# Kernel optimization log

Hardware: AMD Instinct MI355X
Metric: run time of the kernel (lower is better)

## Reference

```python
import jax, jax.numpy as jnp
import numpy as np

N = 50000      # nodes
E = 800000     # edges (avg degree 16)
G = 50         # graphs in batch (1000 nodes each)
D_IN, H, H2, OUT = 8, 128, 64, 1


def setup_inputs() -> dict:
    key = jax.random.key(0)
    ks = jax.random.split(key, 16)
    src = jax.random.randint(ks[0], (E,), 0, N)
    # every node gets at least one in-edge (forward computes 3/in_deg)
    dst = jnp.concatenate([jnp.arange(N), jax.random.randint(ks[1], (E - N,), 0, N)])
    graph_ids = jnp.arange(N) // (N // G)

    def lin(k, fan_in, fan_out):
        return jax.random.normal(k, (fan_in, fan_out), jnp.float32) / np.float32(np.sqrt(fan_in))

    inp = {"src": src, "dst": dst, "graph_ids": graph_ids}
    dims = [(D_IN, H), (H, H), (H, H), (H, H), (H, H)]
    for i, (fi, fo) in enumerate(dims):
        inp[f"W{i+1}"] = lin(ks[2 + i], fi, fo)
        inp[f"b{i+1}"] = jnp.zeros((fo,), jnp.float32)
    inp["lw1"] = lin(ks[8], H, H2)
    inp["lb1"] = jnp.zeros((H2,), jnp.float32)
    inp["lw2"] = lin(ks[9], H2, OUT)
    inp["lb2"] = jnp.zeros((OUT,), jnp.float32)
    return inp


def reference(src, dst, graph_ids, W1, b1, W2, b2, W3, b3, W4, b4, W5, b5, lw1, lb1, lw2, lb2):
    ones_e = jnp.ones((E,), jnp.float32)
    in_deg = jax.ops.segment_sum(ones_e, dst, num_segments=N)   # [N]
    out_deg = jax.ops.segment_sum(ones_e, src, num_segments=N)  # [N]

    # degree features (8 channels)
    h1 = in_deg[:, None]
    h2 = (in_deg > 3.0).astype(jnp.float32)[:, None]
    h3 = 3.0 / h1
    h4 = (in_deg > 4.0).astype(jnp.float32)[:, None]
    h_ = jnp.concatenate([h1, h2, h3, h4, -h1, -h2, -h3, -h4], axis=1)  # [N,8]

    # DGL GraphConv norm='both': clamp degrees to min 1 for normalization
    norm_src = jnp.maximum(out_deg, 1.0) ** -0.5  # [N]
    norm_dst = jnp.maximum(in_deg, 1.0) ** -0.5   # [N]

    def conv(h, W, b):
        m = (h * norm_src[:, None])[src]                        # [E, d] gather
        agg = jax.ops.segment_sum(m, dst, num_segments=N)       # [N, d] scatter-add
        return agg * norm_dst[:, None] @ W + b

    h_co = jax.nn.relu(conv(h_, W1, b1))
    h_co = jax.nn.relu(conv(h_co, W2, b2))
    h_co = jax.nn.relu(conv(h_co, W3, b3))
    h_co = jax.nn.relu(conv(h_co, W4, b4))
    h_co = jax.nn.relu(conv(h_co, W5, b5))                      # [N, H]

    # dgl.mean_nodes: per-graph mean pool
    counts = jax.ops.segment_sum(jnp.ones((N,), jnp.float32), graph_ids, num_segments=G)
    graph_emb = jax.ops.segment_sum(h_co, graph_ids, num_segments=G) / counts[:, None]  # [G, H]

    # dropout layers are identity in eval mode
    h_emb = jax.nn.relu(graph_emb @ lw1 + lb1)
    pred = jax.nn.sigmoid(h_emb @ lw2 + lb2)                    # [G, 1]
    return (pred, graph_emb, h_co)
```

## Files before the change

### kernel.cpp

```cpp
#include <hip/hip_runtime.h>
#include <math.h>

#define N_NODES 50000
#define N_EDGES 800000
#define N_GRAPHS 50
#define HD 128
#define TM 64
#define LDA 68
#define POOL_CHUNK 125
#define SCAN_B 256
#define SCAN_NB ((N_NODES + SCAN_B - 1) / SCAN_B)
#define NB_H 128
#define CH_H (N_EDGES / NB_H)
#define NBIN2 (N_NODES / 2)

__global__ __launch_bounds__(256) void k_hist(const int* __restrict__ src,
                                              const int* __restrict__ dst,
                                              unsigned* __restrict__ part_in,
                                              unsigned* __restrict__ part_out) {
    __shared__ unsigned cnt[NBIN2];
    int t = threadIdx.x, b = blockIdx.x;
    int e0 = b * CH_H;
    for (int j = t; j < NBIN2; j += 256) cnt[j] = 0;
    __syncthreads();
    for (int e = e0 + t; e < e0 + CH_H; e += 256) {
        int i = dst[e];
        atomicAdd(&cnt[i >> 1], 1u << ((i & 1) * 16));
    }
    __syncthreads();
    for (int j = t; j < NBIN2; j += 256) part_in[b * NBIN2 + j] = cnt[j];
    __syncthreads();
    for (int j = t; j < NBIN2; j += 256) cnt[j] = 0;
    __syncthreads();
    for (int e = e0 + t; e < e0 + CH_H; e += 256) {
        int i = src[e];
        atomicAdd(&cnt[i >> 1], 1u << ((i & 1) * 16));
    }
    __syncthreads();
    for (int j = t; j < NBIN2; j += 256) part_out[b * NBIN2 + j] = cnt[j];
}

__global__ void k_dreduce(const unsigned* __restrict__ part_in,
                          const unsigned* __restrict__ part_out,
                          int* __restrict__ deg_in, int* __restrict__ deg_out) {
    int j = blockIdx.x * blockDim.x + threadIdx.x;
    if (j >= NBIN2) return;
    unsigned ilo = 0, ihi = 0, olo = 0, ohi = 0;
#pragma unroll 4
    for (int b = 0; b < NB_H; ++b) {
        unsigned pi = part_in[b * NBIN2 + j];
        unsigned po = part_out[b * NBIN2 + j];
        ilo += pi & 0xFFFFu; ihi += pi >> 16;
        olo += po & 0xFFFFu; ohi += po >> 16;
    }
    ((int2*)deg_in)[j] = make_int2((int)ilo, (int)ihi);
    ((int2*)deg_out)[j] = make_int2((int)olo, (int)ohi);
}

__global__ void k_norms(const int* __restrict__ deg_in, const int* __restrict__ deg_out,
                        const int* __restrict__ gids,
                        float* norm_src, float* norm_dst, int* gcount,
                        float4* __restrict__ feat4) {
    __shared__ int hist[N_GRAPHS];
    int t = threadIdx.x;
    if (t < N_GRAPHS) hist[t] = 0;
    __syncthreads();
    int i = blockIdx.x * blockDim.x + t;
    if (i < N_NODES) {
        float di = (float)deg_in[i];
        float dq = (float)deg_out[i];
        float nd = 1.0f / sqrtf(fmaxf(di, 1.0f));
        float ns = 1.0f / sqrtf(fmaxf(dq, 1.0f));
        norm_dst[i] = nd;
        norm_src[i] = ns;
        float4 f;
        f.x = di * ns;
        f.y = (di > 3.0f) ? ns : 0.0f;
        f.z = (3.0f / di) * ns;
        f.w = (di > 4.0f) ? ns : 0.0f;
        feat4[i] = f;
        atomicAdd(&hist[gids[i]], 1);
    }
    __syncthreads();
    if (t < N_GRAPHS && hist[t] != 0) atomicAdd(&gcount[t], hist[t]);
}

__global__ void k_scan1(const int* __restrict__ deg_in, int* off, int* bsum) {
    __shared__ int sh[SCAN_B];
    int t = threadIdx.x;
    int i = blockIdx.x * SCAN_B + t;
    int v = (i < N_NODES) ? deg_in[i] : 0;
    sh[t] = v;
    __syncthreads();
    for (int o = 1; o < SCAN_B; o <<= 1) {
        int u = (t >= o) ? sh[t - o] : 0;
        __syncthreads();
        sh[t] += u;
        __syncthreads();
    }
    if (i < N_NODES) off[i] = sh[t] - v;
    if (t == SCAN_B - 1) bsum[blockIdx.x] = sh[t];
}

__global__ void k_scan2(int* bsum, int* off) {
    __shared__ int sh[SCAN_B];
    int t = threadIdx.x;
    int v = (t < SCAN_NB) ? bsum[t] : 0;
    sh[t] = v;
    __syncthreads();
    for (int o = 1; o < SCAN_B; o <<= 1) {
        int u = (t >= o) ? sh[t - o] : 0;
        __syncthreads();
        sh[t] += u;
        __syncthreads();
    }
    if (t < SCAN_NB) bsum[t] = sh[t] - v;
    if (t == SCAN_B - 1) off[N_NODES] = sh[t];
}

__global__ void k_scan3(int* off, const int* __restrict__ bsum, int* cursor) {
    int b = blockIdx.x, t = threadIdx.x;
    int i = b * SCAN_B + t;
    if (i < N_NODES) {
        int o = off[i] + bsum[b];
        off[i] = o;
        cursor[i] = o;
    }
}

__global__ void k_scatter(const int* __restrict__ src, const int* __restrict__ dst,
                          int* cursor, int* csr) {
    int e = blockIdx.x * blockDim.x + threadIdx.x;
    if (e < N_EDGES) {
        int p = atomicAdd(&cursor[dst[e]], 1);
        csr[p] = src[e];
    }
}

__global__ void k_agg1(const int* __restrict__ off, const int* __restrict__ csr,
                       const float4* __restrict__ feat4,
                       const float* __restrict__ ndst, float* __restrict__ agg8) {
    int i = blockIdx.x * blockDim.x + threadIdx.x;
    if (i >= N_NODES) return;
    int e0 = off[i], e1 = off[i + 1];
    float a0 = 0.f, a1 = 0.f, a2 = 0.f, a3 = 0.f;
    int e = e0;
    for (; e + 1 < e1; e += 2) {
        float4 f0 = feat4[csr[e]];
        float4 f1 = feat4[csr[e + 1]];
        a0 += f0.x + f1.x; a1 += f0.y + f1.y;
        a2 += f0.z + f1.z; a3 += f0.w + f1.w;
    }
    if (e < e1) {
        float4 f0 = feat4[csr[e]];
        a0 += f0.x; a1 += f0.y; a2 += f0.z; a3 += f0.w;
    }
    float nd = ndst[i];
    a0 *= nd; a1 *= nd; a2 *= nd; a3 *= nd;
    float4* p = (float4*)(agg8 + (size_t)i * 8);
    float4 hi = { a0, a1, a2, a3 };
    float4 lo = { -a0, -a1, -a2, -a3 };
    p[0] = hi;
    p[1] = lo;
}

__global__ void k_gemm1(const float* __restrict__ agg8, const float* __restrict__ W,
                        const float* __restrict__ b, const float* __restrict__ nsrc,
                        float* __restrict__ out) {
    __shared__ float Wsh[8 * 128];
    int t = threadIdx.x;
    for (int i = t; i < 1024; i += 256) Wsh[i] = W[i];
    __syncthreads();
    int row = blockIdx.x * 2 + (t >> 7);
    int j = t & 127;
    if (row >= N_NODES) return;
    const float* a = agg8 + (size_t)row * 8;
    float acc = b[j];
#pragma unroll
    for (int k = 0; k < 8; ++k) acc += a[k] * Wsh[k * 128 + j];
    out[(size_t)row * HD + j] = fmaxf(acc, 0.0f) * nsrc[row];
}

__global__ void k_agg4(const int* __restrict__ off, const int* __restrict__ csr,
                       const float* __restrict__ ndst,
                       const float* __restrict__ h, float* __restrict__ out) {
    int wid = (blockIdx.x * blockDim.x + threadIdx.x) >> 6;
    int lane = threadIdx.x & 63;
    if (wid >= N_NODES) return;
    int half = lane >> 5;
    int q = lane & 31;
    int e0 = off[wid], e1 = off[wid + 1];
    float4 a = { 0.f, 0.f, 0.f, 0.f };
    int e = e0 + half;
    for (; e + 2 < e1; e += 4) {
        int s0 = csr[e], s1 = csr[e + 2];
        float4 v0 = *(const float4*)(h + (size_t)s0 * HD + q * 4);
        float4 v1 = *(const float4*)(h + (size_t)s1 * HD + q * 4);
        a.x += v0.x + v1.x; a.y += v0.y + v1.y;
        a.z += v0.z + v1.z; a.w += v0.w + v1.w;
    }
    if (e < e1) {
        int s0 = csr[e];
        float4 v0 = *(const float4*)(h + (size_t)s0 * HD + q * 4);
        a.x += v0.x; a.y += v0.y; a.z += v0.z; a.w += v0.w;
    }
    a.x += __shfl_xor(a.x, 32);
    a.y += __shfl_xor(a.y, 32);
    a.z += __shfl_xor(a.z, 32);
    a.w += __shfl_xor(a.w, 32);
    if (half == 0) {
        float nd = ndst[wid];
        a.x *= nd; a.y *= nd; a.z *= nd; a.w *= nd;
        *(float4*)(out + (size_t)wid * HD + q * 4) = a;
    }
}

__global__ void k_agg2(const int* __restrict__ off, const int* __restrict__ csr,
                       const float* __restrict__ ndst,
                       const float* __restrict__ h, float* __restrict__ out) {
    int wid = (blockIdx.x * blockDim.x + threadIdx.x) >> 6;
    int lane = threadIdx.x & 63;
    if (wid >= N_NODES) return;
    int e0 = off[wid], e1 = off[wid + 1];
    float a0 = 0.f, a1 = 0.f;
    int e = e0;
    for (; e + 3 < e1; e += 4) {
        int s0 = csr[e], s1 = csr[e + 1], s2 = csr[e + 2], s3 = csr[e + 3];
        float2 v0 = *(const float2*)(h + (size_t)s0 * HD + lane * 2);
        float2 v1 = *(const float2*)(h + (size_t)s1 * HD + lane * 2);
        float2 v2 = *(const float2*)(h + (size_t)s2 * HD + lane * 2);
        float2 v3 = *(const float2*)(h + (size_t)s3 * HD + lane * 2);
        a0 += v0.x + v1.x + v2.x + v3.x;
        a1 += v0.y + v1.y + v2.y + v3.y;
    }
    for (; e < e1; ++e) {
        int s0 = csr[e];
        float2 v0 = *(const float2*)(h + (size_t)s0 * HD + lane * 2);
        a0 += v0.x; a1 += v0.y;
    }
    float nd = ndst[wid];
    float2 o; o.x = a0 * nd; o.y = a1 * nd;
    *(float2*)(out + (size_t)wid * HD + lane * 2) = o;
}

__global__ __launch_bounds__(512) void k_gemm(const float* __restrict__ A,
                                              const float* __restrict__ W,
                                              const float* __restrict__ b,
                                              const float* __restrict__ nsrc,
                                              int premult,
                                              float* __restrict__ out) {
    __shared__ float Wsh[128 * 128];
    __shared__ float Ash[128 * LDA];
    int t = threadIdx.x;
    const float4* W4 = (const float4*)W;
    float4* Wsh4 = (float4*)Wsh;
#pragma unroll
    for (int i = 0; i < 8; ++i) Wsh4[t + i * 512] = W4[t + i * 512];
    int row0 = blockIdx.x * TM;
#pragma unroll
    for (int i = 0; i < 4; ++i) {
        int idx = t + i * 512;
        int r = idx >> 5;
        int q = idx & 31;
        int row = row0 + r;
        if (row >= N_NODES) row = N_NODES - 1;
        float4 v = ((const float4*)(A + (size_t)row * HD))[q];
        Ash[(4 * q + 0) * LDA + r] = v.x;
        Ash[(4 * q + 1) * LDA + r] = v.y;
        Ash[(4 * q + 2) * LDA + r] = v.z;
        Ash[(4 * q + 3) * LDA + r] = v.w;
    }
    __syncthreads();
    int j0 = (t & 31) * 4;
    int r0 = (t >> 5) * 4;
    float4 bv = *(const float4*)(b + j0);
    float acc[4][4];
#pragma unroll
    for (int r = 0; r < 4; ++r) {
        acc[r][0] = bv.x; acc[r][1] = bv.y; acc[r][2] = bv.z; acc[r][3] = bv.w;
    }
#pragma unroll 4
    for (int k = 0; k < 128; ++k) {
        float4 w = *(const float4*)&Wsh[k * 128 + j0];
        float4 a = *(const float4*)&Ash[k * LDA + r0];
        acc[0][0] += a.x * w.x; acc[0][1] += a.x * w.y; acc[0][2] += a.x * w.z; acc[0][3] += a.x * w.w;
        acc[1][0] += a.y * w.x; acc[1][1] += a.y * w.y; acc[1][2] += a.y * w.z; acc[1][3] += a.y * w.w;
        acc[2][0] += a.z * w.x; acc[2][1] += a.z * w.y; acc[2][2] += a.z * w.z; acc[2][3] += a.z * w.w;
        acc[3][0] += a.w * w.x; acc[3][1] += a.w * w.y; acc[3][2] += a.w * w.z; acc[3][3] += a.w * w.w;
    }
#pragma unroll
    for (int r = 0; r < 4; ++r) {
        int row = row0 + r0 + r;
        if (row < N_NODES) {
            float sc = premult ? nsrc[row] : 1.0f;
            float* op = out + (size_t)row * HD + j0;
            float2 o01 = { fmaxf(acc[r][0], 0.f) * sc, fmaxf(acc[r][1], 0.f) * sc };
            float2 o23 = { fmaxf(acc[r][2], 0.f) * sc, fmaxf(acc[r][3], 0.f) * sc };
            *(float2*)op = o01;
            *(float2*)(op + 2) = o23;
        }
    }
}

__global__ void k_pool(const float* __restrict__ hco, const int* __restrict__ gids,
                       float* gsum) {
    int f = threadIdx.x;
    int n0 = blockIdx.x * POOL_CHUNK;
    int g = gids[n0];
    float s = 0.f;
    for (int i = 0; i < POOL_CHUNK; ++i)
        s += hco[(size_t)(n0 + i) * HD + f];
    atomicAdd(&gsum[g * HD + f], s);
}

__global__ void k_head(const float* __restrict__ gsum, const int* __restrict__ gcount,
                       const float* __restrict__ lw1, const float* __restrict__ lb1,
                       const float* __restrict__ lw2, const float* __restrict__ lb2,
                       float* __restrict__ dout) {
    __shared__ float ge[128];
    int g = blockIdx.x, j = threadIdx.x;
    float cnt = (float)gcount[g];
    float g0 = gsum[g * HD + j] / cnt;
    float g1 = gsum[g * HD + 64 + j] / cnt;
    ge[j] = g0; ge[64 + j] = g1;
    dout[N_GRAPHS + g * HD + j] = g0;
    dout[N_GRAPHS + g * HD + 64 + j] = g1;
    __syncthreads();
    float acc = lb1[j];
#pragma unroll 4
    for (int k = 0; k < 128; ++k) acc += ge[k] * lw1[k * 64 + j];
    float he = fmaxf(acc, 0.f);
    float p = he * lw2[j];
#pragma unroll
    for (int o = 32; o > 0; o >>= 1) p += __shfl_down(p, o);
    if (j == 0) dout[g] = 1.0f / (1.0f + expf(-(p + lb2[0])));
}

extern "C" void kernel_launch(void* const* d_in, const int* in_sizes, int n_in,
                              void* d_out, int out_size, void* d_ws, size_t ws_size,
                              hipStream_t stream) {
    const int* src  = (const int*)d_in[0];
    const int* dst  = (const int*)d_in[1];
    const int* gids = (const int*)d_in[2];
    const float* W1 = (const float*)d_in[3];  const float* b1 = (const float*)d_in[4];
    const float* W2 = (const float*)d_in[5];  const float* b2 = (const float*)d_in[6];
    const float* W3 = (const float*)d_in[7];  const float* b3 = (const float*)d_in[8];
    const float* W4 = (const float*)d_in[9];  const float* b4 = (const float*)d_in[10];
    const float* W5 = (const float*)d_in[11]; const float* b5 = (const float*)d_in[12];
    const float* lw1 = (const float*)d_in[13]; const float* lb1 = (const float*)d_in[14];
    const float* lw2 = (const float*)d_in[15]; const float* lb2 = (const float*)d_in[16];
    float* out = (float*)d_out;

    char* ws = (char*)d_ws;
    int*    gcount   = (int*)(ws + 0);
    float*  gsum     = (float*)(ws + 256);
    const size_t ZERO_BYTES = 25856;
    int*    deg_in   = (int*)(ws + 26112);
    int*    deg_out  = (int*)(ws + 226304);
    int*    off      = (int*)(ws + 426496);
    int*    cursor   = (int*)(ws + 626688);
    int*    csr      = (int*)(ws + 826880);
    float*  norm_src = (float*)(ws + 4026880);
    float*  norm_dst = (float*)(ws + 4227072);
    int*    bsum     = (int*)(ws + 4427264);
    float4* feat4    = (float4*)(ws + 4428288);
    float*  aggbuf   = (float*)(ws + 5228544);
    float*  hws      = (float*)(ws + 30828544);
    const size_t WS_NEEDED = 30828544 + 25600000;

    unsigned* part_in  = (unsigned*)aggbuf;
    unsigned* part_out = (unsigned*)aggbuf + NB_H * NBIN2;

    float* hco = out + (N_GRAPHS + N_GRAPHS * HD);
    bool aligned = (ws_size >= WS_NEEDED);
    float* hbuf = aligned ? hws : hco;

    hipMemsetAsync(ws, 0, ZERO_BYTES, stream);

    k_hist<<<NB_H, 256, 0, stream>>>(src, dst, part_in, part_out);
    k_dreduce<<<(NBIN2 + 255) / 256, 256, 0, stream>>>(part_in, part_out,
                                                       deg_in, deg_out);
    k_norms<<<(N_NODES + 255) / 256, 256, 0, stream>>>(deg_in, deg_out, gids,
                                                       norm_src, norm_dst, gcount, feat4);
    k_scan1<<<SCAN_NB, SCAN_B, 0, stream>>>(deg_in, off, bsum);
    k_scan2<<<1, SCAN_B, 0, stream>>>(bsum, off);
    k_scan3<<<SCAN_NB, SCAN_B, 0, stream>>>(off, bsum, cursor);
    k_scatter<<<(N_EDGES + 255) / 256, 256, 0, stream>>>(src, dst, cursor, csr);

    k_agg1<<<(N_NODES + 255) / 256, 256, 0, stream>>>(off, csr, feat4, norm_dst, aggbuf);
    k_gemm1<<<N_NODES / 2, 256, 0, stream>>>(aggbuf, W1, b1, norm_src, hbuf);

    const float* Ws[4] = { W2, W3, W4, W5 };
    const float* bs[4] = { b2, b3, b4, b5 };
    for (int L = 0; L < 4; ++L) {
        if (aligned)
            k_agg4<<<(N_NODES * 64 + 255) / 256, 256, 0, stream>>>(off, csr,
                                                                   norm_dst, hbuf, aggbuf);
        else
            k_agg2<<<(N_NODES * 64 + 255) / 256, 256, 0, stream>>>(off, csr,
                                                                   norm_dst, hbuf, aggbuf);
        float* gout = (L < 3) ? hbuf : hco;
        k_gemm<<<(N_NODES + TM - 1) / TM, 512, 0, stream>>>(aggbuf, Ws[L], bs[L],
                                                            norm_src, (L < 3) ? 1 : 0,
                                                            gout);
    }

    k_pool<<<N_NODES / POOL_CHUNK, 128, 0, stream>>>(hco, gids, gsum);
    k_head<<<N_GRAPHS, 64, 0, stream>>>(gsum, gcount, lw1, lb1, lw2, lb2, out);
}
```

Before: 540.5 us.

## Build CSR from per-block histogram prefix offsets instead of global atomics

The degree-reduction kernel now writes, for each histogram block, an exclusive running prefix of the packed per-node counts back into the partial buffer. A new scatter kernel loads its block's prefix into LDS and uses shared-memory atomics to rank each edge within its destination. This replaces the global-atomic cursor scatter and drops the cursor buffer, and the CSR order becomes deterministic. The gather in the aggregation kernel is also unrolled to four loads in flight per half-wave. Risks: the 16-bit packed running sums overflow if any node's in-degree exceeds 65535, and the scatter now runs on only 128 blocks.

```diff
diff --git a/kernel.cpp b/kernel.cpp
--- a/kernel.cpp
+++ b/kernel.cpp
@@ -40,21 +40,21 @@
     for (int j = t; j < NBIN2; j += 256) part_out[b * NBIN2 + j] = cnt[j];
 }
 
-__global__ void k_dreduce(const unsigned* __restrict__ part_in,
+__global__ void k_dreduce(unsigned* __restrict__ part_in,
                           const unsigned* __restrict__ part_out,
                           int* __restrict__ deg_in, int* __restrict__ deg_out) {
     int j = blockIdx.x * blockDim.x + threadIdx.x;
     if (j >= NBIN2) return;
-    unsigned ilo = 0, ihi = 0, olo = 0, ohi = 0;
-#pragma unroll 4
+    unsigned run_i = 0, run_o = 0;
     for (int b = 0; b < NB_H; ++b) {
         unsigned pi = part_in[b * NBIN2 + j];
         unsigned po = part_out[b * NBIN2 + j];
-        ilo += pi & 0xFFFFu; ihi += pi >> 16;
-        olo += po & 0xFFFFu; ohi += po >> 16;
-    }
-    ((int2*)deg_in)[j] = make_int2((int)ilo, (int)ihi);
-    ((int2*)deg_out)[j] = make_int2((int)olo, (int)ohi);
+        part_in[b * NBIN2 + j] = run_i;
+        run_i += pi;
+        run_o += po;
+    }
+    ((int2*)deg_in)[j] = make_int2((int)(run_i & 0xFFFFu), (int)(run_i >> 16));
+    ((int2*)deg_out)[j] = make_int2((int)(run_o & 0xFFFFu), (int)(run_o >> 16));
 }
 
 __global__ void k_norms(const int* __restrict__ deg_in, const int* __restrict__ deg_out,
@@ -118,22 +118,29 @@
     if (t == SCAN_B - 1) off[N_NODES] = sh[t];
 }
 
-__global__ void k_scan3(int* off, const int* __restrict__ bsum, int* cursor) {
+__global__ void k_scan3(int* off, const int* __restrict__ bsum) {
     int b = blockIdx.x, t = threadIdx.x;
     int i = b * SCAN_B + t;
-    if (i < N_NODES) {
-        int o = off[i] + bsum[b];
-        off[i] = o;
-        cursor[i] = o;
-    }
-}
-
-__global__ void k_scatter(const int* __restrict__ src, const int* __restrict__ dst,
-                          int* cursor, int* csr) {
-    int e = blockIdx.x * blockDim.x + threadIdx.x;
-    if (e < N_EDGES) {
-        int p = atomicAdd(&cursor[dst[e]], 1);
-        csr[p] = src[e];
+    if (i < N_NODES) off[i] += bsum[b];
+}
+
+__global__ __launch_bounds__(256) void k_scatter2(const int* __restrict__ src,
+                                                  const int* __restrict__ dst,
+                                                  const int* __restrict__ off,
+                                                  const unsigned* __restrict__ part_in,
+                                                  int* __restrict__ csr) {
+    __shared__ unsigned cur[NBIN2];
+    int t = threadIdx.x, b = blockIdx.x;
+    const unsigned* base = part_in + (size_t)b * NBIN2;
+    for (int j = t; j < NBIN2; j += 256) cur[j] = base[j];
+    __syncthreads();
+    int e0 = b * CH_H;
+    for (int e = e0 + t; e < e0 + CH_H; e += 256) {
+        int d = dst[e];
+        int sh = (d & 1) * 16;
+        unsigned old = atomicAdd(&cur[d >> 1], 1u << sh);
+        int rank = (int)((old >> sh) & 0xFFFFu);
+        csr[off[d] + rank] = src[e];
     }
 }
 
@@ -181,9 +188,11 @@
     out[(size_t)row * HD + j] = fmaxf(acc, 0.0f) * nsrc[row];
 }
 
-__global__ void k_agg4(const int* __restrict__ off, const int* __restrict__ csr,
-                       const float* __restrict__ ndst,
-                       const float* __restrict__ h, float* __restrict__ out) {
+__global__ __launch_bounds__(256) void k_agg4(const int* __restrict__ off,
+                                              const int* __restrict__ csr,
+                                              const float* __restrict__ ndst,
+                                              const float* __restrict__ h,
+                                              float* __restrict__ out) {
     int wid = (blockIdx.x * blockDim.x + threadIdx.x) >> 6;
     int lane = threadIdx.x & 63;
     if (wid >= N_NODES) return;
@@ -192,14 +201,18 @@
     int e0 = off[wid], e1 = off[wid + 1];
     float4 a = { 0.f, 0.f, 0.f, 0.f };
     int e = e0 + half;
-    for (; e + 2 < e1; e += 4) {
-        int s0 = csr[e], s1 = csr[e + 2];
+    for (; e + 6 < e1; e += 8) {
+        int s0 = csr[e], s1 = csr[e + 2], s2 = csr[e + 4], s3 = csr[e + 6];
         float4 v0 = *(const float4*)(h + (size_t)s0 * HD + q * 4);
         float4 v1 = *(const float4*)(h + (size_t)s1 * HD + q * 4);
-        a.x += v0.x + v1.x; a.y += v0.y + v1.y;
-        a.z += v0.z + v1.z; a.w += v0.w + v1.w;
-    }
-    if (e < e1) {
+        float4 v2 = *(const float4*)(h + (size_t)s2 * HD + q * 4);
+        float4 v3 = *(const float4*)(h + (size_t)s3 * HD + q * 4);
+        a.x += v0.x + v1.x + v2.x + v3.x;
+        a.y += v0.y + v1.y + v2.y + v3.y;
+        a.z += v0.z + v1.z + v2.z + v3.z;
+        a.w += v0.w + v1.w + v2.w + v3.w;
+    }
+    for (; e < e1; e += 2) {
         int s0 = csr[e];
         float4 v0 = *(const float4*)(h + (size_t)s0 * HD + q * 4);
         a.x += v0.x; a.y += v0.y; a.z += v0.z; a.w += v0.w;
@@ -358,7 +371,6 @@
     int*    deg_in   = (int*)(ws + 26112);
     int*    deg_out  = (int*)(ws + 226304);
     int*    off      = (int*)(ws + 426496);
-    int*    cursor   = (int*)(ws + 626688);
     int*    csr      = (int*)(ws + 826880);
     float*  norm_src = (float*)(ws + 4026880);
     float*  norm_dst = (float*)(ws + 4227072);
@@ -384,8 +396,8 @@
                                                        norm_src, norm_dst, gcount, feat4);
     k_scan1<<<SCAN_NB, SCAN_B, 0, stream>>>(deg_in, off, bsum);
     k_scan2<<<1, SCAN_B, 0, stream>>>(bsum, off);
-    k_scan3<<<SCAN_NB, SCAN_B, 0, stream>>>(off, bsum, cursor);
-    k_scatter<<<(N_EDGES + 255) / 256, 256, 0, stream>>>(src, dst, cursor, csr);
+    k_scan3<<<SCAN_NB, SCAN_B, 0, stream>>>(off, bsum);
+    k_scatter2<<<NB_H, 256, 0, stream>>>(src, dst, off, part_in, csr);
 
     k_agg1<<<(N_NODES + 255) / 256, 256, 0, stream>>>(off, csr, feat4, norm_dst, aggbuf);
     k_gemm1<<<N_NODES / 2, 256, 0, stream>>>(aggbuf, W1, b1, norm_src, hbuf);
```

After: 519.7 us. 3.8% less time.
